# Kernel optimization log

Hardware: AMD Instinct MI355X
Metric: run time of the kernel (lower is better)

Reference implementation:

```python
import jax, jax.numpy as jnp
import numpy as np

D_MODEL, HIDDEN, N_EXPERTS, TOP_K = 1024, 2048, 8, 2
RMS_EPS = 1e-6


def setup_inputs() -> dict:
    key = jax.random.key(0)
    ks = jax.random.split(key, 6)
    B, S = 4, 2048
    return {
        "x": jax.random.normal(ks[0], (B, S, D_MODEL), jnp.float32),
        "norm_weight": jnp.ones((D_MODEL,), jnp.float32),
        "gate_w": jax.random.normal(ks[1], (N_EXPERTS, D_MODEL), jnp.float32) * 0.02,
        "w1": jax.random.normal(ks[2], (N_EXPERTS, HIDDEN, D_MODEL), jnp.float32) * 0.02,
        "b1": jnp.zeros((N_EXPERTS, HIDDEN), jnp.float32),
        "w2": jax.random.normal(ks[3], (N_EXPERTS, D_MODEL, HIDDEN), jnp.float32) * 0.02,
        "b2": jnp.zeros((N_EXPERTS, D_MODEL), jnp.float32),
    }


def reference(x, norm_weight, gate_w, w1, b1, w2, b2):
    B, S, D = x.shape
    E = gate_w.shape[0]
    # RMSNorm
    t = x * jax.lax.rsqrt(jnp.mean(x * x, axis=-1, keepdims=True) + RMS_EPS) * norm_weight
    tokens = t.reshape(-1, D)                      # [T, D]
    T = tokens.shape[0]
    # Top-k routing (eval mode: no gate noise)
    gate_logits = tokens @ gate_w.T                # [T, E]
    gate_scores, expert_idx = jax.lax.top_k(gate_logits, TOP_K)
    routing_weights = jax.nn.softmax(gate_scores, axis=-1)  # [T, K]
    # Per-token per-expert combine weight (scatter routing weights into [T, E])
    combine = jnp.zeros((T, E), tokens.dtype).at[
        jnp.arange(T)[:, None], expert_idx
    ].add(routing_weights)
    # Scan over experts; inactive tokens have combine weight 0, matching the
    # masked gather/scatter-add math of the original exactly.
    def body(acc, params):
        W1, B1, W2, B2, c = params                 # c: [T]
        h = jax.nn.gelu(tokens @ W1.T + B1, approximate=False)  # [T, H]
        o = h @ W2.T + B2                          # [T, D]
        return acc + c[:, None] * o, None

    out, _ = jax.lax.scan(body, jnp.zeros_like(tokens), (w1, b1, w2, b2, combine.T))
    return x + out.reshape(B, S, D)
```

## Files before the change

### kernel.cpp

```cpp
#include <hip/hip_runtime.h>
#include <hip/hip_bf16.h>
#include <stdint.h>

#define D_MODEL 1024
#define HIDDEN  2048
#define N_EXP   8
#define T_TOK   8192
#define MAXPOS  17408
#define ROWTILES (MAXPOS/128)

typedef __attribute__((ext_vector_type(4))) float f32x4;
typedef __attribute__((ext_vector_type(8))) short short8v;

__device__ __forceinline__ unsigned short f2bf(float f) {
    union { float f; unsigned int u; } v; v.f = f;
    unsigned int u = v.u;
    unsigned int r = (u + 0x7fffu + ((u >> 16) & 1u)) >> 16;
    return (unsigned short)r;
}
__device__ __forceinline__ float bf2f(unsigned short s) {
    union { unsigned int u; float f; } v; v.u = ((unsigned int)s) << 16;
    return v.f;
}

__device__ __forceinline__ void gload_lds16(const void* g, void* l) {
    __builtin_amdgcn_global_load_lds(
        reinterpret_cast<const __attribute__((address_space(1))) unsigned int*>(
            reinterpret_cast<uintptr_t>(g)),
        reinterpret_cast<__attribute__((address_space(3))) unsigned int*>(
            (uint32_t)reinterpret_cast<uintptr_t>(l)),
        16, 0, 0);
}

__global__ void rms_gate_kernel(const float* __restrict__ x,
                                const float* __restrict__ nw,
                                const float* __restrict__ gw,
                                unsigned short* __restrict__ tb,
                                int* __restrict__ tok_e,
                                float* __restrict__ tok_w) {
    const int wave = threadIdx.x >> 6;
    const int lane = threadIdx.x & 63;
    const int t = blockIdx.x * 4 + wave;

    const float4* xr = (const float4*)(x + (size_t)t * D_MODEL);
    const float4* wr = (const float4*)nw;
    float4 xv[4], wv[4];
    #pragma unroll
    for (int j = 0; j < 4; j++) {
        xv[j] = xr[j * 64 + lane];
        wv[j] = wr[j * 64 + lane];
    }

    float ssq = 0.0f;
    #pragma unroll
    for (int j = 0; j < 4; j++)
        ssq += xv[j].x * xv[j].x + xv[j].y * xv[j].y + xv[j].z * xv[j].z + xv[j].w * xv[j].w;
    #pragma unroll
    for (int off = 32; off; off >>= 1) ssq += __shfl_xor(ssq, off);
    const float scale = rsqrtf(ssq * (1.0f / D_MODEL) + 1e-6f);

    float4 tn[4];
    #pragma unroll
    for (int j = 0; j < 4; j++) {
        tn[j].x = xv[j].x * wv[j].x * scale;
        tn[j].y = xv[j].y * wv[j].y * scale;
        tn[j].z = xv[j].z * wv[j].z * scale;
        tn[j].w = xv[j].w * wv[j].w * scale;
    }

    ushort4* tw = (ushort4*)(tb + (size_t)t * D_MODEL);
    #pragma unroll
    for (int j = 0; j < 4; j++) {
        ushort4 o;
        o.x = f2bf(tn[j].x); o.y = f2bf(tn[j].y);
        o.z = f2bf(tn[j].z); o.w = f2bf(tn[j].w);
        tw[j * 64 + lane] = o;
    }

    float d[8];
    #pragma unroll
    for (int e = 0; e < 8; e++) {
        d[e] = 0.0f;
        #pragma unroll
        for (int j = 0; j < 4; j++) {
            float4 g = ((const float4*)(gw + e * D_MODEL))[j * 64 + lane];
            d[e] += tn[j].x * g.x + tn[j].y * g.y + tn[j].z * g.z + tn[j].w * g.w;
        }
    }
    #pragma unroll
    for (int e = 0; e < 8; e++) {
        #pragma unroll
        for (int off = 32; off; off >>= 1) d[e] += __shfl_xor(d[e], off);
    }

    if (lane == 0) {
        int i0 = 0;
        #pragma unroll
        for (int e = 1; e < 8; e++) if (d[e] > d[i0]) i0 = e;
        int i1 = -1;
        #pragma unroll
        for (int e = 0; e < 8; e++)
            if (e != i0 && (i1 < 0 || d[e] > d[i1])) i1 = e;
        float e1 = expf(d[i1] - d[i0]);
        float w0 = 1.0f / (1.0f + e1);
        ((int2*)tok_e)[t]   = make_int2(i0, i1);
        ((float2*)tok_w)[t] = make_float2(w0, e1 * w0);
    }
}

__global__ void hist_kernel(const int* __restrict__ tok_e, int* __restrict__ counts) {
    __shared__ int lh[8];
    if (threadIdx.x < 8) lh[threadIdx.x] = 0;
    __syncthreads();
    int i = blockIdx.x * 512 + threadIdx.x;
    atomicAdd(&lh[tok_e[i]], 1);
    atomicAdd(&lh[tok_e[i + 256]], 1);
    __syncthreads();
    if (threadIdx.x < 8) atomicAdd(&counts[threadIdx.x], lh[threadIdx.x]);
}

__global__ void scan_fill_kernel(int* __restrict__ perm_tok,
                                 const int* __restrict__ counts,
                                 int* __restrict__ poff, int* __restrict__ pos_ctr) {
    int i = blockIdx.x * 256 + threadIdx.x;
    if (i < MAXPOS) perm_tok[i] = 0;
    if (blockIdx.x == 0 && threadIdx.x == 0) {
        int acc = 0; poff[0] = 0;
        #pragma unroll
        for (int e = 0; e < 8; e++) {
            pos_ctr[e] = 0;
            acc += (counts[e] + 127) & ~127;
            poff[e + 1] = acc;
        }
    }
}

__global__ void scatter_kernel(const int* __restrict__ tok_e,
                               const int* __restrict__ poff, int* __restrict__ pos_ctr,
                               int* __restrict__ perm_tok, int* __restrict__ tok_pos) {
    __shared__ int lh[8], lbase[8];
    if (threadIdx.x < 8) lh[threadIdx.x] = 0;
    __syncthreads();
    int t = blockIdx.x * 256 + threadIdx.x;
    int2 ee = ((const int2*)tok_e)[t];
    int p0 = atomicAdd(&lh[ee.x], 1);
    int p1 = atomicAdd(&lh[ee.y], 1);
    __syncthreads();
    if (threadIdx.x < 8) lbase[threadIdx.x] = atomicAdd(&pos_ctr[threadIdx.x], lh[threadIdx.x]);
    __syncthreads();
    int q0 = poff[ee.x] + lbase[ee.x] + p0;
    int q1 = poff[ee.y] + lbase[ee.y] + p1;
    perm_tok[q0] = t;
    perm_tok[q1] = t;
    ((int2*)tok_pos)[t] = make_int2(q0, q1);
}

__global__ void cvt_bf16_kernel(const float4* __restrict__ in,
                                ushort4* __restrict__ outp, int n4) {
    int i = blockIdx.x * blockDim.x + threadIdx.x;
    if (i >= n4) return;
    float4 v = in[i];
    ushort4 o; o.x = f2bf(v.x); o.y = f2bf(v.y); o.z = f2bf(v.z); o.w = f2bf(v.w);
    outp[i] = o;
}

template <int MODE, int K, int N>
__global__ __launch_bounds__(256) void moe_gemm_kernel(
                                const unsigned short* __restrict__ A,
                                const unsigned short* __restrict__ W,
                                const float* __restrict__ bias,
                                const int* __restrict__ perm_tok,
                                const int* __restrict__ poff,
                                unsigned short* __restrict__ Cout) {
    constexpr int NT = N / 128;
    __shared__ short lds[17408];
    short* Asm = lds;
    short* Bsm = lds + 8192;

    const int nwg = gridDim.x;
    const int cpx = nwg >> 3;
    const int bid = (int)blockIdx.x;
    const int swz = (bid & 7) * cpx + (bid >> 3);

    const int rt = swz / NT, nt = swz % NT;
    const int row_base = rt * 128;
    if (row_base >= poff[8]) return;
    int e = 0;
    while (poff[e + 1] <= row_base) ++e;
    const int n0 = nt * 128;

    const int tid = threadIdx.x;
    const int wave = tid >> 6, lane = tid & 63;
    const int colb = (tid & 7) * 16;
    const int wr = wave >> 1, wc = wave & 1;

    size_t aoff[4], boff[4];
    #pragma unroll
    for (int i = 0; i < 4; i++) {
        int r = row_base + i * 32 + (tid >> 3);
        int arow = (MODE == 1) ? perm_tok[r] : r;
        aoff[i] = (size_t)arow * (K * 2);
        int brow = n0 + i * 32 + (tid >> 3);
        boff[i] = ((size_t)e * N + brow) * (size_t)(K * 2);
    }
    const char* Ab = (const char*)A;
    const char* Wb = (const char*)W;

    f32x4 acc[4][4];
    #pragma unroll
    for (int mi = 0; mi < 4; mi++)
        #pragma unroll
        for (int ni = 0; ni < 4; ni++) acc[mi][ni] = (f32x4)(0.0f);

    for (int k0b = 0; k0b < K * 2; k0b += 128) {
        #pragma unroll
        for (int i = 0; i < 4; i++) {
            gload_lds16(Ab + aoff[i] + k0b + colb, (char*)Asm + i * 4096 + wave * 1024);
            gload_lds16(Wb + boff[i] + k0b + colb, (char*)Bsm + i * 4096 + wave * 1024);
        }
        __syncthreads();
        #pragma unroll
        for (int kk = 0; kk < 2; kk++) {
            short8v af[4], bf[4];
            #pragma unroll
            for (int mi = 0; mi < 4; mi++)
                af[mi] = *(const short8v*)&Asm[(wr * 64 + mi * 16 + (lane & 15)) * 64 + kk * 32 + (lane >> 4) * 8];
            #pragma unroll
            for (int ni = 0; ni < 4; ni++)
                bf[ni] = *(const short8v*)&Bsm[(wc * 64 + ni * 16 + (lane & 15)) * 64 + kk * 32 + (lane >> 4) * 8];
            #pragma unroll
            for (int mi = 0; mi < 4; mi++)
                #pragma unroll
                for (int ni = 0; ni < 4; ni++)
                    acc[mi][ni] = __builtin_amdgcn_mfma_f32_16x16x32_bf16(af[mi], bf[ni], acc[mi][ni], 0, 0, 0);
        }
        __syncthreads();
    }

    #pragma unroll
    for (int mi = 0; mi < 4; mi++) {
        #pragma unroll
        for (int ni = 0; ni < 4; ni++) {
            int lc = wc * 64 + ni * 16 + (lane & 15);
            float bv = bias[e * N + n0 + lc];
            #pragma unroll
            for (int j = 0; j < 4; j++) {
                int lr = wr * 64 + mi * 16 + (lane >> 4) * 4 + j;
                float v = acc[mi][ni][j] + bv;
                if (MODE == 1)
                    v = 0.5f * v * (1.0f + erff(v * 0.70710678118654752f));
                lds[lr * 136 + lc] = (short)f2bf(v);
            }
        }
    }
    __syncthreads();
    {
        const int rr = tid >> 4;
        const int cc = tid & 15;
        #pragma unroll
        for (int p = 0; p < 8; p++) {
            int lr = p * 16 + rr;
            short8v vv = *(const short8v*)&lds[lr * 136 + cc * 8];
            *(short8v*)(Cout + (size_t)(row_base + lr) * N + n0 + cc * 8) = vv;
        }
    }
}

__global__ void combine_kernel(const float* __restrict__ x,
                               const int* __restrict__ tok_pos,
                               const float* __restrict__ tok_w,
                               const unsigned short* __restrict__ obuf,
                               float* __restrict__ out) {
    const int wave = threadIdx.x >> 6;
    const int lane = threadIdx.x & 63;
    const int t = blockIdx.x * 4 + wave;
    int2 pp = ((const int2*)tok_pos)[t];
    float2 ww = ((const float2*)tok_w)[t];
    const float4* xr = (const float4*)(x + (size_t)t * D_MODEL);
    float4* orow = (float4*)(out + (size_t)t * D_MODEL);
    const short4* o0 = (const short4*)(obuf + (size_t)pp.x * D_MODEL);
    const short4* o1 = (const short4*)(obuf + (size_t)pp.y * D_MODEL);
    #pragma unroll
    for (int j = 0; j < 4; j++) {
        int idx = j * 64 + lane;
        float4 xv = xr[idx];
        short4 a = o0[idx];
        short4 b = o1[idx];
        float4 r;
        r.x = xv.x + ww.x * bf2f((unsigned short)a.x) + ww.y * bf2f((unsigned short)b.x);
        r.y = xv.y + ww.x * bf2f((unsigned short)a.y) + ww.y * bf2f((unsigned short)b.y);
        r.z = xv.z + ww.x * bf2f((unsigned short)a.z) + ww.y * bf2f((unsigned short)b.z);
        r.w = xv.w + ww.x * bf2f((unsigned short)a.w) + ww.y * bf2f((unsigned short)b.w);
        orow[idx] = r;
    }
}

extern "C" void kernel_launch(void* const* d_in, const int* in_sizes, int n_in,
                              void* d_out, int out_size, void* d_ws, size_t ws_size,
                              hipStream_t stream) {
    const float* x  = (const float*)d_in[0];
    const float* nw = (const float*)d_in[1];
    const float* gw = (const float*)d_in[2];
    const float* w1 = (const float*)d_in[3];
    const float* b1 = (const float*)d_in[4];
    const float* w2 = (const float*)d_in[5];
    const float* b2 = (const float*)d_in[6];
    float* out = (float*)d_out;
    char* ws = (char*)d_ws;

    size_t off = 0;
    unsigned short* tb   = (unsigned short*)(ws + off); off += (size_t)T_TOK * D_MODEL * 2;
    unsigned short* w1b  = (unsigned short*)(ws + off); off += (size_t)N_EXP * HIDDEN * D_MODEL * 2;
    unsigned short* w2b  = (unsigned short*)(ws + off); off += (size_t)N_EXP * D_MODEL * HIDDEN * 2;
    unsigned short* h    = (unsigned short*)(ws + off); off += (size_t)MAXPOS * HIDDEN * 2;
    unsigned short* obuf = (unsigned short*)(ws + off); off += (size_t)MAXPOS * D_MODEL * 2;
    int*   perm_tok = (int*)(ws + off);   off += MAXPOS * 4;
    int*   tok_e    = (int*)(ws + off);   off += T_TOK * 2 * 4;
    float* tok_w    = (float*)(ws + off); off += T_TOK * 2 * 4;
    int*   tok_pos  = (int*)(ws + off);   off += T_TOK * 2 * 4;
    int*   meta     = (int*)(ws + off);
    int* counts  = meta;
    int* pos_ctr = meta + 8;
    int* poff    = meta + 16;

    hipMemsetAsync(meta, 0, 32, stream);

    rms_gate_kernel<<<T_TOK / 4, 256, 0, stream>>>(x, nw, gw, tb, tok_e, tok_w);

    const int n4 = N_EXP * HIDDEN * D_MODEL / 4;
    cvt_bf16_kernel<<<n4 / 256, 256, 0, stream>>>((const float4*)w1, (ushort4*)w1b, n4);
    cvt_bf16_kernel<<<n4 / 256, 256, 0, stream>>>((const float4*)w2, (ushort4*)w2b, n4);

    hist_kernel<<<32, 256, 0, stream>>>(tok_e, counts);
    scan_fill_kernel<<<MAXPOS / 256, 256, 0, stream>>>(perm_tok, counts, poff, pos_ctr);
    scatter_kernel<<<T_TOK / 256, 256, 0, stream>>>(tok_e, poff, pos_ctr, perm_tok, tok_pos);

    moe_gemm_kernel<1, D_MODEL, HIDDEN><<<ROWTILES * (HIDDEN / 128), 256, 0, stream>>>(
        tb, w1b, b1, perm_tok, poff, h);
    moe_gemm_kernel<2, HIDDEN, D_MODEL><<<ROWTILES * (D_MODEL / 128), 256, 0, stream>>>(
        h, w2b, b2, perm_tok, poff, obuf);

    combine_kernel<<<T_TOK / 4, 256, 0, stream>>>(x, tok_pos, tok_w, obuf, out);
}
```

Before: 384.9 us.

## Enlarge MoE GEMM tiles to 256x256 with double-buffered swizzled LDS

```diff
diff --git a/kernel.cpp b/kernel.cpp
--- a/kernel.cpp
+++ b/kernel.cpp
@@ -6,8 +6,9 @@
 #define HIDDEN  2048
 #define N_EXP   8
 #define T_TOK   8192
-#define MAXPOS  17408
-#define ROWTILES (MAXPOS/128)
+#define BM      256
+#define MAXPOS  (16384 + N_EXP * BM)
+#define ROWT    (MAXPOS / BM)
 
 typedef __attribute__((ext_vector_type(4))) float f32x4;
 typedef __attribute__((ext_vector_type(8))) short short8v;
@@ -129,7 +130,7 @@
         #pragma unroll
         for (int e = 0; e < 8; e++) {
             pos_ctr[e] = 0;
-            acc += (counts[e] + 127) & ~127;
+            acc += (counts[e] + (BM - 1)) & ~(BM - 1);
             poff[e + 1] = acc;
         }
     }
@@ -164,105 +165,149 @@
     outp[i] = o;
 }
 
+
+#define STAGE_ALL(BUF, K0) do { \
+    gload_lds16(gb[0][0] + (K0), lds + (BUF)*65536 + 32768 + (w*16)*128); \
+    gload_lds16(gb[0][1] + (K0), lds + (BUF)*65536 + 32768 + (w*16 + 8)*128); \
+    gload_lds16(gb[1][0] + (K0), lds + (BUF)*65536 + 32768 + (128 + w*16)*128); \
+    gload_lds16(gb[1][1] + (K0), lds + (BUF)*65536 + 32768 + (128 + w*16 + 8)*128); \
+    gload_lds16(ga[0] + (K0), lds + (BUF)*65536 + rsA[0]*128); \
+    gload_lds16(ga[1] + (K0), lds + (BUF)*65536 + rsA[1]*128); \
+    gload_lds16(ga[2] + (K0), lds + (BUF)*65536 + rsA[2]*128); \
+    gload_lds16(ga[3] + (K0), lds + (BUF)*65536 + rsA[3]*128); \
+} while (0)
+
 template <int MODE, int K, int N>
-__global__ __launch_bounds__(256) void moe_gemm_kernel(
-                                const unsigned short* __restrict__ A,
-                                const unsigned short* __restrict__ W,
-                                const float* __restrict__ bias,
-                                const int* __restrict__ perm_tok,
-                                const int* __restrict__ poff,
-                                unsigned short* __restrict__ Cout) {
-    constexpr int NT = N / 128;
-    __shared__ short lds[17408];
-    short* Asm = lds;
-    short* Bsm = lds + 8192;
+__global__ __launch_bounds__(512) void moe_gemm_kernel(
+        const unsigned short* __restrict__ A,
+        const unsigned short* __restrict__ W,
+        const float* __restrict__ bias,
+        const int* __restrict__ perm_tok,
+        const int* __restrict__ poff,
+        unsigned short* __restrict__ Cout) {
+    constexpr int NT  = N / 256;
+    constexpr int K2  = K * 2;
+    constexpr int NTK = K / 64;
+    __shared__ __align__(16) char lds[131072];
 
     const int nwg = gridDim.x;
     const int cpx = nwg >> 3;
     const int bid = (int)blockIdx.x;
-    const int swz = (bid & 7) * cpx + (bid >> 3);
-
-    const int rt = swz / NT, nt = swz % NT;
-    const int row_base = rt * 128;
+    const int swzb = (bid & 7) * cpx + (bid >> 3);
+    const int rt = swzb / NT, nt = swzb % NT;
+    const int row_base = rt * BM;
     if (row_base >= poff[8]) return;
     int e = 0;
     while (poff[e + 1] <= row_base) ++e;
-    const int n0 = nt * 128;
+    const int n0 = nt * 256;
 
     const int tid = threadIdx.x;
-    const int wave = tid >> 6, lane = tid & 63;
-    const int colb = (tid & 7) * 16;
-    const int wr = wave >> 1, wc = wave & 1;
-
-    size_t aoff[4], boff[4];
-    #pragma unroll
-    for (int i = 0; i < 4; i++) {
-        int r = row_base + i * 32 + (tid >> 3);
-        int arow = (MODE == 1) ? perm_tok[r] : r;
-        aoff[i] = (size_t)arow * (K * 2);
-        int brow = n0 + i * 32 + (tid >> 3);
-        boff[i] = ((size_t)e * N + brow) * (size_t)(K * 2);
-    }
+    const int w = tid >> 6, l = tid & 63;
+    const int wr = w >> 2, wc = w & 3;
+    const int cswz = ((l & 7) * 16) ^ (l & 32);
+
     const char* Ab = (const char*)A;
     const char* Wb = (const char*)W;
-
-    f32x4 acc[4][4];
-    #pragma unroll
-    for (int mi = 0; mi < 4; mi++)
+    const char* ga[4];
+    const char* gb[2][2];
+    int rsA[4];
+    #pragma unroll
+    for (int s = 0; s < 4; s++) {
+        int rstart = (w < 4) ? (s * 32 + w * 8) : (128 + s * 32 + (w - 4) * 8);
+        rsA[s] = rstart;
+        int r = row_base + rstart + (l >> 3);
+        size_t arow = (MODE == 1) ? (size_t)perm_tok[r] : (size_t)r;
+        ga[s] = Ab + arow * K2 + cswz;
+    }
+    #pragma unroll
+    for (int g = 0; g < 2; g++)
+        #pragma unroll
+        for (int j = 0; j < 2; j++) {
+            int r = g * 128 + w * 16 + j * 8 + (l >> 3);
+            gb[g][j] = Wb + ((size_t)e * N + n0 + r) * K2 + cswz;
+        }
+
+    const int aRow = (wr * 128 + (l & 15)) * 128;
+    const int bRow = (wc * 64 + (l & 15)) * 128;
+    const int csw0 = (((l >> 4) * 16)      ) ^ ((l & 4) << 3);
+    const int csw1 = (64 + ((l >> 4) * 16) ) ^ ((l & 4) << 3);
+
+    f32x4 acc[8][4];
+    #pragma unroll
+    for (int mi = 0; mi < 8; mi++)
         #pragma unroll
         for (int ni = 0; ni < 4; ni++) acc[mi][ni] = (f32x4)(0.0f);
-
-    for (int k0b = 0; k0b < K * 2; k0b += 128) {
-        #pragma unroll
-        for (int i = 0; i < 4; i++) {
-            gload_lds16(Ab + aoff[i] + k0b + colb, (char*)Asm + i * 4096 + wave * 1024);
-            gload_lds16(Wb + boff[i] + k0b + colb, (char*)Bsm + i * 4096 + wave * 1024);
+    short8v bfr[4][2];
+
+    STAGE_ALL(0, 0);
+    __syncthreads();
+
+    int cur = 0;
+    #pragma unroll 1
+    for (int t = 0; t < NTK; ++t) {
+        if (t + 1 < NTK) {
+            const int kn = (t + 1) * 128;
+            STAGE_ALL(1 - cur, kn);
+        }
+        const char* BL = lds + cur * 65536 + 32768 + bRow;
+        #pragma unroll
+        for (int ni = 0; ni < 4; ni++) {
+            bfr[ni][0] = *(const short8v*)(BL + ni * 2048 + csw0);
+            bfr[ni][1] = *(const short8v*)(BL + ni * 2048 + csw1);
+        }
+        const char* AL = lds + cur * 65536 + aRow;
+        #pragma unroll
+        for (int q = 0; q < 4; q++) {
+            short8v af0 = *(const short8v*)(AL + q * 4096 + csw0);
+            short8v af1 = *(const short8v*)(AL + q * 4096 + csw1);
+            short8v af2 = *(const short8v*)(AL + q * 4096 + 2048 + csw0);
+            short8v af3 = *(const short8v*)(AL + q * 4096 + 2048 + csw1);
+            #pragma unroll
+            for (int ni = 0; ni < 4; ni++) {
+                acc[2*q][ni]   = __builtin_amdgcn_mfma_f32_16x16x32_bf16(af0, bfr[ni][0], acc[2*q][ni],   0, 0, 0);
+                acc[2*q][ni]   = __builtin_amdgcn_mfma_f32_16x16x32_bf16(af1, bfr[ni][1], acc[2*q][ni],   0, 0, 0);
+                acc[2*q+1][ni] = __builtin_amdgcn_mfma_f32_16x16x32_bf16(af2, bfr[ni][0], acc[2*q+1][ni], 0, 0, 0);
+                acc[2*q+1][ni] = __builtin_amdgcn_mfma_f32_16x16x32_bf16(af3, bfr[ni][1], acc[2*q+1][ni], 0, 0, 0);
+            }
         }
         __syncthreads();
-        #pragma unroll
-        for (int kk = 0; kk < 2; kk++) {
-            short8v af[4], bf[4];
+        cur ^= 1;
+    }
+
+    short* sl = (short*)lds;
+    #pragma unroll
+    for (int h = 0; h < 2; h++) {
+        if ((wc >> 1) == h) {
             #pragma unroll
-            for (int mi = 0; mi < 4; mi++)
-                af[mi] = *(const short8v*)&Asm[(wr * 64 + mi * 16 + (lane & 15)) * 64 + kk * 32 + (lane >> 4) * 8];
+            for (int mi = 0; mi < 8; mi++) {
+                #pragma unroll
+                for (int ni = 0; ni < 4; ni++) {
+                    int gcol = wc * 64 + ni * 16 + (l & 15);
+                    int lc   = gcol - h * 128;
+                    float bv = bias[e * N + n0 + gcol];
+                    #pragma unroll
+                    for (int j = 0; j < 4; j++) {
+                        int lr = wr * 128 + mi * 16 + (l >> 4) * 4 + j;
+                        float v = acc[mi][ni][j] + bv;
+                        if (MODE == 1)
+                            v = 0.5f * v * (1.0f + erff(v * 0.70710678118654752f));
+                        sl[lr * 136 + lc] = (short)f2bf(v);
+                    }
+                }
+            }
+        }
+        __syncthreads();
+        {
+            const int rr = tid >> 4;
+            const int cc = tid & 15;
             #pragma unroll
-            for (int ni = 0; ni < 4; ni++)
-                bf[ni] = *(const short8v*)&Bsm[(wc * 64 + ni * 16 + (lane & 15)) * 64 + kk * 32 + (lane >> 4) * 8];
-            #pragma unroll
-            for (int mi = 0; mi < 4; mi++)
-                #pragma unroll
-                for (int ni = 0; ni < 4; ni++)
-                    acc[mi][ni] = __builtin_amdgcn_mfma_f32_16x16x32_bf16(af[mi], bf[ni], acc[mi][ni], 0, 0, 0);
+            for (int p = 0; p < 8; p++) {
+                int lr = p * 32 + rr;
+                short8v v = *(const short8v*)&sl[lr * 136 + cc * 8];
+                *(short8v*)(Cout + (size_t)(row_base + lr) * N + n0 + h * 128 + cc * 8) = v;
+            }
         }
         __syncthreads();
-    }
-
-    #pragma unroll
-    for (int mi = 0; mi < 4; mi++) {
-        #pragma unroll
-        for (int ni = 0; ni < 4; ni++) {
-            int lc = wc * 64 + ni * 16 + (lane & 15);
-            float bv = bias[e * N + n0 + lc];
-            #pragma unroll
-            for (int j = 0; j < 4; j++) {
-                int lr = wr * 64 + mi * 16 + (lane >> 4) * 4 + j;
-                float v = acc[mi][ni][j] + bv;
-                if (MODE == 1)
-                    v = 0.5f * v * (1.0f + erff(v * 0.70710678118654752f));
-                lds[lr * 136 + lc] = (short)f2bf(v);
-            }
-        }
-    }
-    __syncthreads();
-    {
-        const int rr = tid >> 4;
-        const int cc = tid & 15;
-        #pragma unroll
-        for (int p = 0; p < 8; p++) {
-            int lr = p * 16 + rr;
-            short8v vv = *(const short8v*)&lds[lr * 136 + cc * 8];
-            *(short8v*)(Cout + (size_t)(row_base + lr) * N + n0 + cc * 8) = vv;
-        }
     }
 }
 
@@ -335,9 +380,9 @@
     scan_fill_kernel<<<MAXPOS / 256, 256, 0, stream>>>(perm_tok, counts, poff, pos_ctr);
     scatter_kernel<<<T_TOK / 256, 256, 0, stream>>>(tok_e, poff, pos_ctr, perm_tok, tok_pos);
 
-    moe_gemm_kernel<1, D_MODEL, HIDDEN><<<ROWTILES * (HIDDEN / 128), 256, 0, stream>>>(
+    moe_gemm_kernel<1, D_MODEL, HIDDEN><<<ROWT * (HIDDEN / 256), 512, 0, stream>>>(
         tb, w1b, b1, perm_tok, poff, h);
-    moe_gemm_kernel<2, HIDDEN, D_MODEL><<<ROWTILES * (D_MODEL / 128), 256, 0, stream>>>(
+    moe_gemm_kernel<2, HIDDEN, D_MODEL><<<ROWT * (D_MODEL / 256), 512, 0, stream>>>(
         h, w2b, b2, perm_tok, poff, obuf);
 
     combine_kernel<<<T_TOK / 4, 256, 0, stream>>>(x, tok_pos, tok_w, obuf, out);
```

Result: no change. 381.8 us (-0.8%).
